# Kernel tuning notes

Hardware: AMD Instinct MI355X
Metric: run time of the kernel (lower is better)

## Reference

```python
import jax, jax.numpy as jnp
import numpy as np

R_GAS = 8.314

def _lin(x, W, b):
    return x @ W.T + b

def _lstm_layer(x, Wih, Whh, bih, bhh):
    # x: [B, T, D]; torch gate order i,f,g,o
    B = x.shape[0]
    H = Whh.shape[1]
    def step(carry, xt):
        h, c = carry
        gates = xt @ Wih.T + bih + h @ Whh.T + bhh
        i, f, g, o = jnp.split(gates, 4, axis=-1)
        c = jax.nn.sigmoid(f) * c + jax.nn.sigmoid(i) * jnp.tanh(g)
        h = jax.nn.sigmoid(o) * jnp.tanh(c)
        return (h, c), h
    h0 = jnp.zeros((B, H), x.dtype)
    (_, _), hs = jax.lax.scan(step, (h0, h0), jnp.swapaxes(x, 0, 1))
    return jnp.swapaxes(hs, 0, 1)  # [B, T, H]

def setup_inputs() -> dict:
    key = jax.random.key(0)
    ks = iter(jax.random.split(key, 40))
    H, D, P, S = 64, 2, 32, 3
    B, T = 256, 2048
    def w(shape, scale=0.1):
        return (jax.random.normal(next(ks), shape, dtype=jnp.float32) * scale)
    inp = {
        'time_series': jax.random.normal(next(ks), (B, T, D), dtype=jnp.float32),
        'static_features': jax.random.normal(next(ks), (B, S), dtype=jnp.float32),
        # LSTM layer 0 and 1 (torch nn.LSTM param layout)
        'lstm_Wih0': w((4 * H, D)), 'lstm_Whh0': w((4 * H, H)),
        'lstm_bih0': w((4 * H,)),  'lstm_bhh0': w((4 * H,)),
        'lstm_Wih1': w((4 * H, H)), 'lstm_Whh1': w((4 * H, H)),
        'lstm_bih1': w((4 * H,)),  'lstm_bhh1': w((4 * H,)),
        # state_extractor: H -> H//2 -> H//2
        'se_W1': w((H // 2, H)), 'se_b1': w((H // 2,)),
        'se_W2': w((H // 2, H // 2)), 'se_b2': w((H // 2,)),
        # physics_branch: S -> P -> P//2 -> 2
        'pb_W1': w((P, S)), 'pb_b1': w((P,)),
        'pb_W2': w((P // 2, P)), 'pb_b2': w((P // 2,)),
        'pb_W3': w((2, P // 2)), 'pb_b3': w((2,)),
        # degradation_rate_predictor: (H//2 + 1 + 2) -> 64 -> 32 -> 1
        'dr_W1': w((64, H // 2 + 3)), 'dr_b1': w((64,)),
        'dr_W2': w((32, 64)), 'dr_b2': w((32,)),
        'dr_W3': w((1, 32)), 'dr_b3': w((1,)),
        # rul_predictor: (H//2 + 1) -> 32 -> 1
        'rul_W1': w((32, H // 2 + 1)), 'rul_b1': w((32,)),
        'rul_W2': w((1, 32)), 'rul_b2': w((1,)),
    }
    return inp

def reference(time_series, static_features,
              lstm_Wih0, lstm_Whh0, lstm_bih0, lstm_bhh0,
              lstm_Wih1, lstm_Whh1, lstm_bih1, lstm_bhh1,
              se_W1, se_b1, se_W2, se_b2,
              pb_W1, pb_b1, pb_W2, pb_b2, pb_W3, pb_b3,
              dr_W1, dr_b1, dr_W2, dr_b2, dr_W3, dr_b3,
              rul_W1, rul_b1, rul_W2, rul_b2):
    B, T, _ = time_series.shape
    # 2-layer LSTM (dropout inactive at inference)
    h1 = _lstm_layer(time_series, lstm_Wih0, lstm_Whh0, lstm_bih0, lstm_bhh0)
    lstm_out = _lstm_layer(h1, lstm_Wih1, lstm_Whh1, lstm_bih1, lstm_bhh1)  # [B,T,H]
    # state extractor, vectorized over time
    system_states = _lin(jax.nn.relu(_lin(lstm_out, se_W1, se_b1)), se_W2, se_b2)  # [B,T,H/2]
    # physics branch -> Ea, log_A
    p = jax.nn.relu(_lin(static_features, pb_W1, pb_b1))
    p = jax.nn.relu(_lin(p, pb_W2, pb_b2))
    physics_params = _lin(p, pb_W3, pb_b3)  # [B,2]
    Ea = physics_params[:, 0:1]
    log_A = physics_params[:, 1:2]
    A = jnp.exp(log_A)
    temperatures = time_series[:, :, 0:1]                 # [B,T,1]
    temps_K = temperatures + 273.15
    Ea_J = (Ea * 1000.0)[:, None, :]                      # [B,1,1]
    arrhenius_rate = A[:, None, :] * jnp.exp(-Ea_J / (R_GAS * temps_K))  # [B,T,1]
    # degradation rate predictor, vectorized (no sequential dependency)
    EaL = jnp.broadcast_to(Ea[:, None, :], (B, T, 1))
    logAL = jnp.broadcast_to(log_A[:, None, :], (B, T, 1))
    rate_in = jnp.concatenate([system_states, temperatures, EaL, logAL], axis=-1)
    r = jax.nn.relu(_lin(rate_in, dr_W1, dr_b1))
    r = jax.nn.relu(_lin(r, dr_W2, dr_b2))
    degradation_rates = _lin(r, dr_W3, dr_b3)             # [B,T,1]
    # sequential health recurrence (dt=1)
    combined = 0.7 * degradation_rates + 0.3 * arrhenius_rate
    def step(h, c):
        h = jnp.clip(h - c, 0.0, 1.0)
        return h, h
    h0 = jnp.ones((B, 1), time_series.dtype)
    _, hs = jax.lax.scan(step, h0, jnp.swapaxes(combined, 0, 1))
    health = jnp.swapaxes(hs, 0, 1)                       # [B,T,1]
    # rul predictor, vectorized
    rul_in = jnp.concatenate([system_states, health], axis=-1)
    q = jax.nn.relu(_lin(rul_in, rul_W1, rul_b1))
    rul = jnp.maximum(_lin(q, rul_W2, rul_b2), 0.0)       # [B,T,1]
    return rul, degradation_rates, health
```

## Files before the change

kernel.cpp:

```cpp
#include <hip/hip_runtime.h>


#define Bn 256
#define Tn 2048
#define NT 512
#define NI 134

typedef _Float16 h2 __attribute__((ext_vector_type(2)));
union HU { int i; h2 h; };

__device__ __forceinline__ h2 I2H(int v) { HU u; u.i = v; return u.h; }
__device__ __forceinline__ h2 F2H2(float a, float b) { h2 r; r.x = (_Float16)a; r.y = (_Float16)b; return r; }
__device__ __forceinline__ float rcpf_(float x) { return __builtin_amdgcn_rcpf(x); }
__device__ __forceinline__ float sigf_(float x) { return rcpf_(1.f + __expf(-x)); }
__device__ __forceinline__ float tanhf2_(float x) {
    float e = __expf(2.0f * x);
    return 1.0f - 2.0f * rcpf_(e + 1.0f);
}
__device__ __forceinline__ void dot2(float& acc, h2 w, h2 x) {
    asm("v_dot2_f32_f16 %0, %1, %2, %0" : "+v"(acc) : "v"(w), "v"(x));
}
#define DPPF(v, ctrl) __int_as_float(__builtin_amdgcn_update_dpp(0, __float_as_int(v), (ctrl), 0xF, 0xF, true))
#define LGKM0() asm volatile("s_waitcnt lgkmcnt(0)" ::: "memory")
#define UNP4(h, o, r) { h[(o)] = I2H((r).x); h[(o)+1] = I2H((r).y); h[(o)+2] = I2H((r).z); h[(o)+3] = I2H((r).w); }

__device__ __forceinline__ float wsum64_(float v) {
    v += DPPF(v, 0xB1); v += DPPF(v, 0x4E);
    v += __shfl_xor(v, 4); v += __shfl_xor(v, 8);
    v += __shfl_xor(v, 16); v += __shfl_xor(v, 32);
    return v;
}

__global__ __launch_bounds__(512, 1)
void fused_rul_kernel(
    const float* __restrict__ ts,   const float* __restrict__ sf,
    const float* __restrict__ Wih0, const float* __restrict__ Whh0,
    const float* __restrict__ bih0, const float* __restrict__ bhh0,
    const float* __restrict__ Wih1, const float* __restrict__ Whh1,
    const float* __restrict__ bih1, const float* __restrict__ bhh1,
    const float* __restrict__ seW1, const float* __restrict__ seb1,
    const float* __restrict__ seW2, const float* __restrict__ seb2,
    const float* __restrict__ pbW1, const float* __restrict__ pbb1,
    const float* __restrict__ pbW2, const float* __restrict__ pbb2,
    const float* __restrict__ pbW3, const float* __restrict__ pbb3,
    const float* __restrict__ drW1, const float* __restrict__ drb1,
    const float* __restrict__ drW2, const float* __restrict__ drb2,
    const float* __restrict__ drW3, const float* __restrict__ drb3,
    const float* __restrict__ ruW1, const float* __restrict__ rub1,
    const float* __restrict__ ruW2, const float* __restrict__ rub2,
    float* __restrict__ out)
{
    const int tid  = threadIdx.x;
    const int b    = blockIdx.x;
    const int lane = tid & 63;
    const int w    = tid >> 6;

    __shared__ __align__(16) _Float16 h0r[64][64];
    __shared__ __align__(16) _Float16 h1r[64][64];
    __shared__ __align__(16) float4   g1r[32][64];
    __shared__ __align__(16) _Float16 ssb[64][32];
    __shared__ __align__(16) _Float16 se1b[4][32];
    __shared__ __align__(16) _Float16 dr1b[4][64];
    __shared__ float degb[32];
    __shared__ float hltb[32];
    __shared__ float phys_s[4];

    const float* tsb = ts + (size_t)b * Tn * 2;
    float* outR = out + (size_t)b * Tn;
    float* outD = out + (size_t)Bn * Tn + (size_t)b * Tn;
    float* outH = out + 2 * (size_t)Bn * Tn + (size_t)b * Tn;

    if (w == 0) {
        h2 wf[128]; float b0[4], wx[4], wy[4];
        #pragma unroll
        for (int g = 0; g < 4; ++g) {
            const int row = (g << 6) + lane;
            const float* r = Whh0 + row * 64;
            #pragma unroll
            for (int k = 0; k < 32; ++k) wf[g * 32 + k] = F2H2(r[2 * k], r[2 * k + 1]);
            b0[g] = bih0[row] + bhh0[row];
            wx[g] = Wih0[row * 2]; wy[g] = Wih0[row * 2 + 1];
        }
        h2 hv[32];
        #pragma unroll
        for (int k = 0; k < 32; ++k) hv[k] = F2H2(0.f, 0.f);
        float c0 = 0.f;
        __syncthreads();
        for (int I = 0; I < NI; ++I) {
            const int base = I << 4;
            if (base < Tn) {
                float2 xp = make_float2(0.f, 0.f);
                if (lane < 16) xp = *(const float2*)(tsb + 2 * (base + lane));
                #pragma unroll 1
                for (int j = 0; j < 16; ++j) {
                    const int u = base + j;
                    float a0 = 0, a1 = 0, a2 = 0, a3 = 0, a4 = 0, a5 = 0, a6 = 0, a7 = 0;
                    #pragma unroll
                    for (int k = 0; k < 16; ++k) {
                        dot2(a0, wf[k],       hv[k]); dot2(a4, wf[16 + k],  hv[16 + k]);
                        dot2(a1, wf[32 + k],  hv[k]); dot2(a5, wf[48 + k],  hv[16 + k]);
                        dot2(a2, wf[64 + k],  hv[k]); dot2(a6, wf[80 + k],  hv[16 + k]);
                        dot2(a3, wf[96 + k],  hv[k]); dot2(a7, wf[112 + k], hv[16 + k]);
                    }
                    float sx = __shfl(xp.x, j), sy = __shfl(xp.y, j);
                    float pi = a0 + a4 + b0[0] + wx[0] * sx + wy[0] * sy;
                    float pf = a1 + a5 + b0[1] + wx[1] * sx + wy[1] * sy;
                    float pg = a2 + a6 + b0[2] + wx[2] * sx + wy[2] * sy;
                    float po = a3 + a7 + b0[3] + wx[3] * sx + wy[3] * sy;
                    float ai = sigf_(pi), af = sigf_(pf), ag = tanhf2_(pg), ao = sigf_(po);
                    c0 = fmaf(af, c0, ai * ag);
                    float h0n = ao * tanhf2_(c0);
                    h0r[u & 63][lane] = (_Float16)h0n;
                    LGKM0();
                    const int4* rp = (const int4*)&h0r[u & 63][0];
                    int4 r0 = rp[0], r1 = rp[1], r2 = rp[2], r3 = rp[3];
                    int4 r4 = rp[4], r5 = rp[5], r6 = rp[6], r7 = rp[7];
                    UNP4(hv, 0, r0);  UNP4(hv, 4, r1);  UNP4(hv, 8, r2);  UNP4(hv, 12, r3);
                    UNP4(hv, 16, r4); UNP4(hv, 20, r5); UNP4(hv, 24, r6); UNP4(hv, 28, r7);
                }
            }
            __syncthreads();
        }
    } else if (w == 1) {
        h2 wf[128];
        #pragma unroll
        for (int g = 0; g < 4; ++g) {
            const float* r = Wih1 + ((g << 6) + lane) * 64;
            #pragma unroll
            for (int k = 0; k < 32; ++k) wf[g * 32 + k] = F2H2(r[2 * k], r[2 * k + 1]);
        }
        __syncthreads();
        for (int I = 0; I < NI; ++I) {
            const int tb = (I << 4) - 16;
            if (tb >= 0 && tb < Tn) {
                #pragma unroll 1
                for (int j = 0; j < 16; ++j) {
                    const int t = tb + j;
                    const int4* rp = (const int4*)&h0r[t & 63][0];
                    int4 r0 = rp[0], r1 = rp[1], r2 = rp[2], r3 = rp[3];
                    int4 r4 = rp[4], r5 = rp[5], r6 = rp[6], r7 = rp[7];
                    h2 hv[32];
                    UNP4(hv, 0, r0);  UNP4(hv, 4, r1);  UNP4(hv, 8, r2);  UNP4(hv, 12, r3);
                    UNP4(hv, 16, r4); UNP4(hv, 20, r5); UNP4(hv, 24, r6); UNP4(hv, 28, r7);
                    float a0 = 0, a1 = 0, a2 = 0, a3 = 0, a4 = 0, a5 = 0, a6 = 0, a7 = 0;
                    #pragma unroll
                    for (int k = 0; k < 16; ++k) {
                        dot2(a0, wf[k],       hv[k]); dot2(a4, wf[16 + k],  hv[16 + k]);
                        dot2(a1, wf[32 + k],  hv[k]); dot2(a5, wf[48 + k],  hv[16 + k]);
                        dot2(a2, wf[64 + k],  hv[k]); dot2(a6, wf[80 + k],  hv[16 + k]);
                        dot2(a3, wf[96 + k],  hv[k]); dot2(a7, wf[112 + k], hv[16 + k]);
                    }
                    g1r[t & 31][lane] = make_float4(a0 + a4, a1 + a5, a2 + a6, a3 + a7);
                }
            }
            __syncthreads();
        }
    } else if (w == 2) {
        h2 wf[128]; float b1[4];
        #pragma unroll
        for (int g = 0; g < 4; ++g) {
            const int row = (g << 6) + lane;
            const float* r = Whh1 + row * 64;
            #pragma unroll
            for (int k = 0; k < 32; ++k) wf[g * 32 + k] = F2H2(r[2 * k], r[2 * k + 1]);
            b1[g] = bih1[row] + bhh1[row];
        }
        h2 hv[32];
        #pragma unroll
        for (int k = 0; k < 32; ++k) hv[k] = F2H2(0.f, 0.f);
        float c1 = 0.f;
        __syncthreads();
        for (int I = 0; I < NI; ++I) {
            const int tb = (I << 4) - 32;
            if (tb >= 0 && tb < Tn) {
                #pragma unroll 1
                for (int j = 0; j < 16; ++j) {
                    const int t = tb + j;
                    float4 p = g1r[t & 31][lane];
                    float a0 = 0, a1 = 0, a2 = 0, a3 = 0, a4 = 0, a5 = 0, a6 = 0, a7 = 0;
                    #pragma unroll
                    for (int k = 0; k < 16; ++k) {
                        dot2(a0, wf[k],       hv[k]); dot2(a4, wf[16 + k],  hv[16 + k]);
                        dot2(a1, wf[32 + k],  hv[k]); dot2(a5, wf[48 + k],  hv[16 + k]);
                        dot2(a2, wf[64 + k],  hv[k]); dot2(a6, wf[80 + k],  hv[16 + k]);
                        dot2(a3, wf[96 + k],  hv[k]); dot2(a7, wf[112 + k], hv[16 + k]);
                    }
                    float pi = p.x + a0 + a4 + b1[0];
                    float pf = p.y + a1 + a5 + b1[1];
                    float pg = p.z + a2 + a6 + b1[2];
                    float po = p.w + a3 + a7 + b1[3];
                    float ai = sigf_(pi), af = sigf_(pf), ag = tanhf2_(pg), ao = sigf_(po);
                    c1 = fmaf(af, c1, ai * ag);
                    float h1n = ao * tanhf2_(c1);
                    h1r[t & 63][lane] = (_Float16)h1n;
                    LGKM0();
                    const int4* rp = (const int4*)&h1r[t & 63][0];
                    int4 r0 = rp[0], r1 = rp[1], r2 = rp[2], r3 = rp[3];
                    int4 r4 = rp[4], r5 = rp[5], r6 = rp[6], r7 = rp[7];
                    UNP4(hv, 0, r0);  UNP4(hv, 4, r1);  UNP4(hv, 8, r2);  UNP4(hv, 12, r3);
                    UNP4(hv, 16, r4); UNP4(hv, 20, r5); UNP4(hv, 24, r6); UNP4(hv, 28, r7);
                }
            }
            __syncthreads();
        }
    } else if (w == 3) {
        if (lane == 0) {
            float p1[32];
            for (int o = 0; o < 32; ++o) {
                float a = pbb1[o];
                for (int k = 0; k < 3; ++k) a += pbW1[o * 3 + k] * sf[b * 3 + k];
                p1[o] = fmaxf(a, 0.f);
            }
            float p2[16];
            for (int o = 0; o < 16; ++o) {
                float a = pbb2[o];
                for (int k = 0; k < 32; ++k) a += pbW2[o * 32 + k] * p1[k];
                p2[o] = fmaxf(a, 0.f);
            }
            float Ea = pbb3[0], lA = pbb3[1];
            for (int k = 0; k < 16; ++k) { Ea += pbW3[k] * p2[k]; lA += pbW3[16 + k] * p2[k]; }
            phys_s[0] = __expf(lA);
            phys_s[1] = -Ea * 1000.0f / 8.314f;
            phys_s[2] = Ea;
            phys_s[3] = lA;
        }
        float hst = 1.0f;
        __syncthreads();
        for (int I = 0; I < NI; ++I) {
            const int t0s = (I << 4) - 80;
            if (t0s >= 0 && t0s < Tn) {
                const int t = lane;
                const float Af = phys_s[0], ne = phys_s[1];
                float a_ = 0.f, l_ = -1e30f, u_ = 1e30f;
                if (t < 16) {
                    float dg = degb[(t0s + t) & 31];
                    float tK = tsb[2 * (t0s + t)] + 273.15f;
                    float arr = Af * __expf(ne * rcpf_(tK));
                    a_ = -(0.7f * dg + 0.3f * arr);
                    l_ = 0.f; u_ = 1.f;
                }
                #pragma unroll
                for (int d = 1; d < 16; d <<= 1) {
                    float pa = __shfl_up(a_, d);
                    float pl = __shfl_up(l_, d);
                    float pu = __shfl_up(u_, d);
                    if (t >= d && t < 16) {
                        float na = pa + a_;
                        float nl = fminf(fmaxf(pl + a_, l_), u_);
                        float nu = fminf(fmaxf(pu + a_, l_), u_);
                        a_ = na; l_ = nl; u_ = nu;
                    }
                }
                float hval = fminf(fmaxf(hst + a_, l_), u_);
                if (t < 16) { hltb[(t0s + t) & 31] = hval; outH[t0s + t] = hval; }
                hst = __shfl(hval, 15);
            }
            __syncthreads();
        }
    } else {
        const int ew = w - 4, jj = lane & 31, hh = lane >> 5;
        h2 w1h[16], w2h[8], wd1h[16], wd2h[16], wr1h[8];
        float wt0, wt1, wt2, bb1, seb1r, seb2r, bb2, w3r, whc, brD, w2rD, drb3r, rub2r;
        {
            const float* r = seW1 + jj * 64 + hh * 32;
            #pragma unroll
            for (int k = 0; k < 16; ++k) w1h[k] = F2H2(r[2 * k], r[2 * k + 1]);
            r = seW2 + jj * 32 + hh * 16;
            #pragma unroll
            for (int k = 0; k < 8; ++k) w2h[k] = F2H2(r[2 * k], r[2 * k + 1]);
            r = drW1 + lane * 35;
            #pragma unroll
            for (int k = 0; k < 16; ++k) wd1h[k] = F2H2(r[2 * k], r[2 * k + 1]);
            wt0 = r[32]; wt1 = r[33]; wt2 = r[34];
            r = drW2 + jj * 64 + hh * 32;
            #pragma unroll
            for (int k = 0; k < 16; ++k) wd2h[k] = F2H2(r[2 * k], r[2 * k + 1]);
            r = ruW1 + jj * 33 + hh * 16;
            #pragma unroll
            for (int k = 0; k < 8; ++k) wr1h[k] = F2H2(r[2 * k], r[2 * k + 1]);
            seb1r = seb1[jj]; seb2r = seb2[jj];
            bb1 = drb1[lane]; bb2 = drb2[jj]; w3r = drW3[jj];
            whc = ruW1[jj * 33 + 32]; brD = rub1[jj]; w2rD = ruW2[jj];
            drb3r = drb3[0]; rub2r = rub2[0];
        }
        __syncthreads();
        for (int I = 0; I < NI; ++I) {
            const int Abase = (I << 4) - 48;
            const int Bbase = (I << 4) - 64;
            const int Dbase = (I << 4) - 96;
            float tpre[4];
            if (Bbase >= 0 && Bbase < Tn) {
                #pragma unroll
                for (int i = 0; i < 4; ++i) tpre[i] = tsb[2 * (Bbase + (ew << 2) + i)];
            }
            if (Abase >= 0 && Abase < Tn) {
                #pragma unroll 1
                for (int i = 0; i < 4; ++i) {
                    const int pos = Abase + (ew << 2) + i;
                    const int slot = pos & 63;
                    const int4* hp = (const int4*)(&h1r[slot][hh * 32]);
                    int4 q0 = hp[0], q1 = hp[1], q2 = hp[2], q3 = hp[3];
                    h2 hv16[16];
                    UNP4(hv16, 0, q0); UNP4(hv16, 4, q1); UNP4(hv16, 8, q2); UNP4(hv16, 12, q3);
                    float acc = 0.f;
                    #pragma unroll
                    for (int k = 0; k < 16; ++k) dot2(acc, w1h[k], hv16[k]);
                    acc += __shfl_xor(acc, 32);
                    float se1v = fmaxf(acc + seb1r, 0.f);
                    if (hh == 0) se1b[ew][jj] = (_Float16)se1v;
                    LGKM0();
                    const int4* sp = (const int4*)(&se1b[ew][hh * 16]);
                    int4 s0 = sp[0], s1 = sp[1];
                    h2 sv[8];
                    UNP4(sv, 0, s0); UNP4(sv, 4, s1);
                    float a2 = 0.f;
                    #pragma unroll
                    for (int k = 0; k < 8; ++k) dot2(a2, w2h[k], sv[k]);
                    a2 += __shfl_xor(a2, 32);
                    if (hh == 0) ssb[slot][jj] = (_Float16)(a2 + seb2r);
                }
            }
            if (Bbase >= 0 && Bbase < Tn) {
                const float ea_ = phys_s[2], la_ = phys_s[3];
                #pragma unroll 1
                for (int i = 0; i < 4; ++i) {
                    const int pos = Bbase + (ew << 2) + i;
                    const int slot = pos & 63;
                    const int4* xp = (const int4*)(&ssb[slot][0]);
                    int4 x0 = xp[0], x1 = xp[1], x2 = xp[2], x3 = xp[3];
                    h2 xv[16];
                    UNP4(xv, 0, x0); UNP4(xv, 4, x1); UNP4(xv, 8, x2); UNP4(xv, 12, x3);
                    float acc = 0.f;
                    #pragma unroll
                    for (int k = 0; k < 16; ++k) dot2(acc, wd1h[k], xv[k]);
                    acc += wt0 * tpre[i] + wt1 * ea_ + wt2 * la_;
                    dr1b[ew][lane] = (_Float16)fmaxf(acc + bb1, 0.f);
                    LGKM0();
                    const int4* dp = (const int4*)(&dr1b[ew][hh * 32]);
                    int4 d0 = dp[0], d1 = dp[1], d2 = dp[2], d3 = dp[3];
                    h2 dv[16];
                    UNP4(dv, 0, d0); UNP4(dv, 4, d1); UNP4(dv, 8, d2); UNP4(dv, 12, d3);
                    float a2 = 0.f;
                    #pragma unroll
                    for (int k = 0; k < 16; ++k) dot2(a2, wd2h[k], dv[k]);
                    a2 += __shfl_xor(a2, 32);
                    float tt = w3r * fmaxf(a2 + bb2, 0.f);
                    float sum = wsum64_(tt);
                    float deg = 0.5f * sum + drb3r;
                    if (lane == 0) { degb[pos & 31] = deg; outD[pos] = deg; }
                }
            }
            if (Dbase >= 0 && Dbase < Tn) {
                #pragma unroll 1
                for (int i = 0; i < 4; ++i) {
                    const int pos = Dbase + (ew << 2) + i;
                    const int slot = pos & 63;
                    const int4* xp = (const int4*)(&ssb[slot][hh * 16]);
                    int4 x0 = xp[0], x1 = xp[1];
                    h2 xv[8];
                    UNP4(xv, 0, x0); UNP4(xv, 4, x1);
                    float acc = 0.f;
                    #pragma unroll
                    for (int k = 0; k < 8; ++k) dot2(acc, wr1h[k], xv[k]);
                    acc += __shfl_xor(acc, 32);
                    float a = acc + brD + whc * hltb[pos & 31];
                    float pp = w2rD * fmaxf(a, 0.f);
                    float sum = wsum64_(pp);
                    if (lane == 0) outR[pos] = fmaxf(0.5f * sum + rub2r, 0.f);
                }
            }
            __syncthreads();
        }
    }
}

extern "C" void kernel_launch(void* const* d_in, const int* in_sizes, int n_in,
                              void* d_out, int out_size, void* d_ws, size_t ws_size,
                              hipStream_t stream) {
    const float* ts   = (const float*)d_in[0];
    const float* sf   = (const float*)d_in[1];
    const float* Wih0 = (const float*)d_in[2];
    const float* Whh0 = (const float*)d_in[3];
    const float* bih0 = (const float*)d_in[4];
    const float* bhh0 = (const float*)d_in[5];
    const float* Wih1 = (const float*)d_in[6];
    const float* Whh1 = (const float*)d_in[7];
    const float* bih1 = (const float*)d_in[8];
    const float* bhh1 = (const float*)d_in[9];
    const float* seW1 = (const float*)d_in[10];
    const float* seb1 = (const float*)d_in[11];
    const float* seW2 = (const float*)d_in[12];
    const float* seb2 = (const float*)d_in[13];
    const float* pbW1 = (const float*)d_in[14];
    const float* pbb1 = (const float*)d_in[15];
    const float* pbW2 = (const float*)d_in[16];
    const float* pbb2 = (const float*)d_in[17];
    const float* pbW3 = (const float*)d_in[18];
    const float* pbb3 = (const float*)d_in[19];
    const float* drW1 = (const float*)d_in[20];
    const float* drb1 = (const float*)d_in[21];
    const float* drW2 = (const float*)d_in[22];
    const float* drb2 = (const float*)d_in[23];
    const float* drW3 = (const float*)d_in[24];
    const float* drb3 = (const float*)d_in[25];
    const float* ruW1 = (const float*)d_in[26];
    const float* rub1 = (const float*)d_in[27];
    const float* ruW2 = (const float*)d_in[28];
    const float* rub2 = (const float*)d_in[29];
    float* out = (float*)d_out;

    fused_rul_kernel<<<dim3(Bn), dim3(NT), 0, stream>>>(
        ts, sf, Wih0, Whh0, bih0, bhh0, Wih1, Whh1, bih1, bhh1,
        seW1, seb1, seW2, seb2, pbW1, pbb1, pbW2, pbb2, pbW3, pbb3,
        drW1, drb1, drW2, drb2, drW3, drb3, ruW1, rub1, ruW2, rub2, out);
}
```

Measured before the change: 1.145 ms.

## Unroll recurrent loops, prefetch gate inputs, use readlane, rebalance epilogue warps

Unrolls the per-timestep loops of the three LSTM waves by two and prefetches the next timestep's layer-1 input-gate values from LDS. Replaces the cross-lane shuffle that broadcasts the time-series input with a scalar readlane. It also splits the 16 positions per block unevenly across the four epilogue waves (2/6/2/6) instead of 4 each, presumably to balance load against waves that share a SIMD with the LSTM waves. Unrolling raises register pressure in waves that already hold 128 packed weight registers.

```diff
diff --git a/kernel.cpp b/kernel.cpp
--- a/kernel.cpp
+++ b/kernel.cpp
@@ -19,6 +19,9 @@
 }
 __device__ __forceinline__ void dot2(float& acc, h2 w, h2 x) {
     asm("v_dot2_f32_f16 %0, %1, %2, %0" : "+v"(acc) : "v"(w), "v"(x));
+}
+__device__ __forceinline__ float rdlane_(float v, int l) {
+    return __int_as_float(__builtin_amdgcn_readlane(__float_as_int(v), l));
 }
 #define DPPF(v, ctrl) __int_as_float(__builtin_amdgcn_update_dpp(0, __float_as_int(v), (ctrl), 0xF, 0xF, true))
 #define LGKM0() asm volatile("s_waitcnt lgkmcnt(0)" ::: "memory")
@@ -91,7 +94,7 @@
             if (base < Tn) {
                 float2 xp = make_float2(0.f, 0.f);
                 if (lane < 16) xp = *(const float2*)(tsb + 2 * (base + lane));
-                #pragma unroll 1
+                #pragma unroll 2
                 for (int j = 0; j < 16; ++j) {
                     const int u = base + j;
                     float a0 = 0, a1 = 0, a2 = 0, a3 = 0, a4 = 0, a5 = 0, a6 = 0, a7 = 0;
@@ -102,7 +105,7 @@
                         dot2(a2, wf[64 + k],  hv[k]); dot2(a6, wf[80 + k],  hv[16 + k]);
                         dot2(a3, wf[96 + k],  hv[k]); dot2(a7, wf[112 + k], hv[16 + k]);
                     }
-                    float sx = __shfl(xp.x, j), sy = __shfl(xp.y, j);
+                    float sx = rdlane_(xp.x, j), sy = rdlane_(xp.y, j);
                     float pi = a0 + a4 + b0[0] + wx[0] * sx + wy[0] * sy;
                     float pf = a1 + a5 + b0[1] + wx[1] * sx + wy[1] * sy;
                     float pg = a2 + a6 + b0[2] + wx[2] * sx + wy[2] * sy;
@@ -133,7 +136,7 @@
         for (int I = 0; I < NI; ++I) {
             const int tb = (I << 4) - 16;
             if (tb >= 0 && tb < Tn) {
-                #pragma unroll 1
+                #pragma unroll 2
                 for (int j = 0; j < 16; ++j) {
                     const int t = tb + j;
                     const int4* rp = (const int4*)&h0r[t & 63][0];
@@ -173,10 +176,12 @@
         for (int I = 0; I < NI; ++I) {
             const int tb = (I << 4) - 32;
             if (tb >= 0 && tb < Tn) {
-                #pragma unroll 1
+                float4 pcur = g1r[tb & 31][lane];
+                #pragma unroll 2
                 for (int j = 0; j < 16; ++j) {
                     const int t = tb + j;
-                    float4 p = g1r[t & 31][lane];
+                    float4 pnext = pcur;
+                    if (j < 15) pnext = g1r[(t + 1) & 31][lane];
                     float a0 = 0, a1 = 0, a2 = 0, a3 = 0, a4 = 0, a5 = 0, a6 = 0, a7 = 0;
                     #pragma unroll
                     for (int k = 0; k < 16; ++k) {
@@ -185,10 +190,10 @@
                         dot2(a2, wf[64 + k],  hv[k]); dot2(a6, wf[80 + k],  hv[16 + k]);
                         dot2(a3, wf[96 + k],  hv[k]); dot2(a7, wf[112 + k], hv[16 + k]);
                     }
-                    float pi = p.x + a0 + a4 + b1[0];
-                    float pf = p.y + a1 + a5 + b1[1];
-                    float pg = p.z + a2 + a6 + b1[2];
-                    float po = p.w + a3 + a7 + b1[3];
+                    float pi = pcur.x + a0 + a4 + b1[0];
+                    float pf = pcur.y + a1 + a5 + b1[1];
+                    float pg = pcur.z + a2 + a6 + b1[2];
+                    float po = pcur.w + a3 + a7 + b1[3];
                     float ai = sigf_(pi), af = sigf_(pf), ag = tanhf2_(pg), ao = sigf_(po);
                     c1 = fmaf(af, c1, ai * ag);
                     float h1n = ao * tanhf2_(c1);
@@ -199,6 +204,7 @@
                     int4 r4 = rp[4], r5 = rp[5], r6 = rp[6], r7 = rp[7];
                     UNP4(hv, 0, r0);  UNP4(hv, 4, r1);  UNP4(hv, 8, r2);  UNP4(hv, 12, r3);
                     UNP4(hv, 16, r4); UNP4(hv, 20, r5); UNP4(hv, 24, r6); UNP4(hv, 28, r7);
+                    pcur = pnext;
                 }
             }
             __syncthreads();
@@ -259,6 +265,8 @@
         }
     } else {
         const int ew = w - 4, jj = lane & 31, hh = lane >> 5;
+        const int eoff = (ew == 0) ? 0 : (ew == 1) ? 2 : (ew == 2) ? 8 : 10;
+        const int ecnt = (ew & 1) ? 6 : 2;
         h2 w1h[16], w2h[8], wd1h[16], wd2h[16], wr1h[8];
         float wt0, wt1, wt2, bb1, seb1r, seb2r, bb2, w3r, whc, brD, w2rD, drb3r, rub2r;
         {
@@ -288,15 +296,17 @@
             const int Abase = (I << 4) - 48;
             const int Bbase = (I << 4) - 64;
             const int Dbase = (I << 4) - 96;
-            float tpre[4];
+            float tpre[6];
             if (Bbase >= 0 && Bbase < Tn) {
                 #pragma unroll
-                for (int i = 0; i < 4; ++i) tpre[i] = tsb[2 * (Bbase + (ew << 2) + i)];
+                for (int i = 0; i < 6; ++i)
+                    if (i < ecnt) tpre[i] = tsb[2 * (Bbase + eoff + i)];
             }
             if (Abase >= 0 && Abase < Tn) {
                 #pragma unroll 1
-                for (int i = 0; i < 4; ++i) {
-                    const int pos = Abase + (ew << 2) + i;
+                for (int i = 0; i < 6; ++i) {
+                    if (i >= ecnt) break;
+                    const int pos = Abase + eoff + i;
                     const int slot = pos & 63;
                     const int4* hp = (const int4*)(&h1r[slot][hh * 32]);
                     int4 q0 = hp[0], q1 = hp[1], q2 = hp[2], q3 = hp[3];
@@ -323,8 +333,9 @@
             if (Bbase >= 0 && Bbase < Tn) {
                 const float ea_ = phys_s[2], la_ = phys_s[3];
                 #pragma unroll 1
-                for (int i = 0; i < 4; ++i) {
-                    const int pos = Bbase + (ew << 2) + i;
+                for (int i = 0; i < 6; ++i) {
+                    if (i >= ecnt) break;
+                    const int pos = Bbase + eoff + i;
                     const int slot = pos & 63;
                     const int4* xp = (const int4*)(&ssb[slot][0]);
                     int4 x0 = xp[0], x1 = xp[1], x2 = xp[2], x3 = xp[3];
@@ -352,8 +363,9 @@
             }
             if (Dbase >= 0 && Dbase < Tn) {
                 #pragma unroll 1
-                for (int i = 0; i < 4; ++i) {
-                    const int pos = Dbase + (ew << 2) + i;
+                for (int i = 0; i < 6; ++i) {
+                    if (i >= ecnt) break;
+                    const int pos = Dbase + eoff + i;
                     const int slot = pos & 63;
                     const int4* xp = (const int4*)(&ssb[slot][hh * 16]);
                     int4 x0 = xp[0], x1 = xp[1];
```

Result: slower. 1.361 ms (+18.8%).
